# Kernel tuning notes

Hardware: AMD Instinct MI355X
Metric: run time of the kernel (lower is better)

## Reference

```python
import jax, jax.numpy as jnp
import numpy as np

PATCH = 16
HIDDEN = 1024
NUM_HEADS = 16
HEAD_DIM = HIDDEN // NUM_HEADS


def sinusoidal_pe(n, d):
    # standard transformer sinusoidal positional encoding, shape [n, d]
    pos = np.arange(n, dtype=np.float32)[:, None]
    i = np.arange(0, d, 2, dtype=np.float32)[None, :]
    ang = pos / np.power(10000.0, i / d)
    pe = np.zeros((n, d), dtype=np.float32)
    pe[:, 0::2] = np.sin(ang)
    pe[:, 1::2] = np.cos(ang)
    return jnp.asarray(pe)


def patch_embed(x, w, b):
    # Conv2d(kernel=stride=PATCH) == non-overlapping patch GEMM
    B, C, H, W = x.shape
    hp, wp = H // PATCH, W // PATCH
    xp = x.reshape(B, C, hp, PATCH, wp, PATCH)
    t = jnp.einsum('bchpwq,dcpq->bhwd', xp, w)  # [B, hp, wp, D]
    return t.reshape(B, hp * wp, -1) + b        # [B, N, D]


def _fit(x, w, b):
    t = patch_embed(x, w, b)
    t = t + sinusoidal_pe(t.shape[1], t.shape[2])
    B, N, _ = t.shape
    return t.reshape(B, N, NUM_HEADS, HEAD_DIM).transpose(0, 2, 1, 3)  # [B,H,N,hd]


def setup_inputs() -> dict:
    key = jax.random.key(0)
    ks = jax.random.split(key, 9)
    B, C, H, W = 16, 3, 512, 512
    return {
        'q_img': jax.random.normal(ks[0], (B, C, H, W), jnp.float32),
        'k_img': jax.random.normal(ks[1], (B, C, H, W), jnp.float32),
        'v_img': jax.random.normal(ks[2], (B, C, H, W), jnp.float32),
        'wq': jax.random.normal(ks[3], (HIDDEN, C, PATCH, PATCH), jnp.float32) * 0.02,
        'bq': jax.random.normal(ks[4], (HIDDEN,), jnp.float32) * 0.02,
        'wk': jax.random.normal(ks[5], (HIDDEN, C, PATCH, PATCH), jnp.float32) * 0.02,
        'bk': jax.random.normal(ks[6], (HIDDEN,), jnp.float32) * 0.02,
        'wv': jax.random.normal(ks[7], (HIDDEN, C, PATCH, PATCH), jnp.float32) * 0.02,
        'bv': jax.random.normal(ks[8], (HIDDEN,), jnp.float32) * 0.02,
    }


def reference(q_img, k_img, v_img, wq, bq, wk, bk, wv, bv):
    q = _fit(q_img, wq, bq)  # [B,H,N,hd]
    k = _fit(k_img, wk, bk)
    v = _fit(v_img, wv, bv)
    q = jax.nn.softmax(q, axis=-1)   # softmax over head_dim
    k = jax.nn.softmax(k, axis=-2)   # softmax over tokens
    scores = jnp.einsum('bhnd,bhne->bhde', k, v)   # k^T v : [B,H,hd,hd]
    ctx = jnp.einsum('bhnd,bhde->bhne', q, scores)  # [B,H,N,hd]
    B, h, N, hd = ctx.shape
    return ctx.transpose(0, 2, 1, 3).reshape(B, N, h * hd)  # [B,N,hidden]
```

## Files before the change

### kernel.cpp

```cpp
#include <hip/hip_runtime.h>
#include <hip/hip_bf16.h>


typedef float  f32x4  __attribute__((ext_vector_type(4)));
typedef __bf16 bf16x8 __attribute__((ext_vector_type(8)));

#define LN10000 9.210340371976184f

__device__ __forceinline__ unsigned short f2bf_bits(float f){
  union { float f; unsigned u; } a; a.f = f;
  unsigned r = a.u + 0x7FFFu + ((a.u >> 16) & 1u);
  return (unsigned short)(r >> 16);
}

__device__ __forceinline__ void gload16(const void* g, void* l){
  __builtin_amdgcn_global_load_lds((__attribute__((address_space(1))) void*)g,
                                   (__attribute__((address_space(3))) void*)l,
                                   16, 0, 0);
}


__global__ __launch_bounds__(256) void k_prep_w(
    const float* __restrict__ wq, const float* __restrict__ wk,
    const float* __restrict__ wv, unsigned short* __restrict__ wbf)
{
  int i = blockIdx.x*256 + threadIdx.x;
  if (i >= 589824) return;
  int z = i / 196608;
  int r = i - z*196608;
  const float* src = (z==0) ? wq : (z==1 ? wk : wv);
  f32x4 v = ((const f32x4*)src)[r];
  unsigned lo = (unsigned)f2bf_bits(v[0]) | ((unsigned)f2bf_bits(v[1]) << 16);
  unsigned hh = (unsigned)f2bf_bits(v[2]) | ((unsigned)f2bf_bits(v[3]) << 16);
  ((uint2*)wbf)[i] = make_uint2(lo, hh);
}

__global__ __launch_bounds__(256) void k_prep_pe(float* __restrict__ pe)
{
  int i = blockIdx.x*256 + threadIdx.x;
  if (i >= 1048576) return;
  int n = i >> 10, dd = i & 1023;
  float ex  = (float)(dd & ~1) * (1.0f/1024.0f);
  float ang = (float)n * expf(-LN10000 * ex);
  pe[i] = (dd & 1) ? cosf(ang) : sinf(ang);
}


__global__ __launch_bounds__(256, 2) void k_embed(
    const float* __restrict__ xq, const float* __restrict__ xk,
    const float* __restrict__ xv, const unsigned short* __restrict__ wbf,
    const float* __restrict__ bq, const float* __restrict__ bk,
    const float* __restrict__ bv, const float* __restrict__ pe,
    float* __restrict__ t_ws)
{
  __shared__ __align__(16) float          ldsA[128*64];
  __shared__ __align__(16) unsigned short ldsB[128*64];

  const int tid = threadIdx.x;
  int flat = blockIdx.x + (blockIdx.y << 3) + (blockIdx.z << 10);
  int orig = (flat & 7)*384 + (flat >> 3);
  const int z   = orig >> 10;
  const int rem = orig & 1023;
  const int m0  = (rem >> 3) * 128;
  const int d0  = (rem & 7) * 128;

  const float* x = (z==0) ? xq : (z==1 ? xk : xv);
  const unsigned short* wz = wbf + z*786432;
  const float* bias = (z==0) ? bq : (z==1 ? bk : bv);
  float* tout = t_ws + (size_t)z*16777216u;

  int aRow[8], aKK[8];
#pragma unroll
  for (int i=0;i<8;i++){
    int L   = i*4096 + tid*16;
    int row = L >> 8;
    int U   = L ^ ((row & 7) << 4);
    aKK[i]  = (U >> 2) & 63;
    int m   = m0 + row;
    int bimg = m >> 10, nt = m & 1023;
    aRow[i] = bimg*786432 + (nt>>5)*8192 + (nt&31)*16;
  }
  int bOff[4];
#pragma unroll
  for (int i=0;i<4;i++){
    int L   = i*4096 + tid*16;
    int row = L >> 7;
    int U   = L ^ ((row & 7) << 4);
    bOff[i] = (d0 + row)*768 + ((U >> 1) & 63);
  }

  const int lane = tid & 63;
  const int wid  = tid >> 6;
  const int ln   = lane & 15, hi4 = lane >> 4;
  const int wm   = wid >> 1,  wn  = wid & 1;

  f32x4 acc[4][4] = {};
  char* ldsAc = (char*)ldsA;
  char* ldsBc = (char*)ldsB;

  for (int ks=0; ks<12; ++ks){
#pragma unroll
    for (int i=0;i<8;i++){
      int k   = ks*64 + aKK[i];
      int c   = k >> 8, rem2 = k & 255;
      int goff = aRow[i] + c*262144 + (rem2>>4)*512 + (rem2 & 15);
      gload16(x + goff, ldsAc + i*4096 + wid*1024);
    }
#pragma unroll
    for (int i=0;i<4;i++){
      gload16(wz + bOff[i] + ks*64, ldsBc + i*4096 + wid*1024);
    }
    __syncthreads();

#pragma unroll
    for (int kc=0; kc<2; ++kc){
      bf16x8 af[4], bfr[4];
#pragma unroll
      for (int mi=0;mi<4;mi++){
        int row  = wm*64 + mi*16 + ln;
        int swz  = (row & 7) << 4;
        int base = row*256 + kc*128 + hi4*32;
        f32x4 lo = *(const f32x4*)(ldsAc + ( base        ^ swz));
        f32x4 hh = *(const f32x4*)(ldsAc + ((base + 16)  ^ swz));
        bf16x8 t;
        t[0]=(__bf16)lo[0]; t[1]=(__bf16)lo[1]; t[2]=(__bf16)lo[2]; t[3]=(__bf16)lo[3];
        t[4]=(__bf16)hh[0]; t[5]=(__bf16)hh[1]; t[6]=(__bf16)hh[2]; t[7]=(__bf16)hh[3];
        af[mi] = t;
      }
#pragma unroll
      for (int ni=0;ni<4;ni++){
        int row  = wn*64 + ni*16 + ln;
        int swz  = (row & 7) << 4;
        int base = row*128 + kc*64 + hi4*16;
        bfr[ni] = *(const bf16x8*)(ldsBc + (base ^ swz));
      }
#pragma unroll
      for (int mi=0;mi<4;mi++)
#pragma unroll
        for (int ni=0;ni<4;ni++)
          acc[mi][ni] = __builtin_amdgcn_mfma_f32_16x16x32_bf16(
              af[mi], bfr[ni], acc[mi][ni], 0, 0, 0);
    }
    __syncthreads();
  }

#pragma unroll
  for (int ni=0;ni<4;ni++){
    int dd = d0 + wn*64 + ni*16 + ln;
    float bv_ = bias[dd];
#pragma unroll
    for (int mi=0;mi<4;mi++){
#pragma unroll
      for (int r=0;r<4;r++){
        int m    = m0 + wm*64 + mi*16 + hi4*4 + r;
        int ntok = m & 1023;
        tout[(size_t)m*1024 + dd] = acc[mi][ni][r] + bv_ + pe[ntok*1024 + dd];
      }
    }
  }
}


__global__ __launch_bounds__(256) void k_scores(
    const float* __restrict__ t_ws, float* __restrict__ scoresRaw)
{
  __shared__ __align__(16) float lds[4][4096];
  __shared__ float ksumLds[4][64];

  const int tid = threadIdx.x;
  const int bh  = blockIdx.x;
  const int b   = bh >> 4, h = bh & 15;
  const float* kbase = t_ws + 16777216u + (size_t)b*1048576u + h*64;
  const float* vbase = t_ws + 33554432u + (size_t)b*1048576u + h*64;

  const int dq = tid & 15, eg = (tid>>4) & 3, npart = tid >> 6;
  const int r0   = tid >> 4;
  const int dcol = (tid & 15) * 4;

#define STAGE(BUF, CH) do{                                                \
    _Pragma("unroll")                                                     \
    for (int i=0;i<4;i++){                                                \
      int row = r0 + 16*i;                                                \
      size_t g = (size_t)((CH)*64 + row)*1024 + dcol;                     \
      f32x4 k4 = *(const f32x4*)(kbase + g);                              \
      f32x4 v4 = *(const f32x4*)(vbase + g);                              \
      f32x4 e;                                                            \
      e[0]=__expf(k4[0]); e[1]=__expf(k4[1]);                             \
      e[2]=__expf(k4[2]); e[3]=__expf(k4[3]);                             \
      *(f32x4*)(&lds[BUF][row*64 + dcol])     = e;                        \
      *(f32x4*)(&lds[2+(BUF)][row*64 + dcol]) = v4;                       \
    } }while(0)

  float acc[4][16] = {};
  float kp[4] = {0.f,0.f,0.f,0.f};

  STAGE(0, 0);
  __syncthreads();
  for (int ch=0; ch<16; ++ch){
    int cur = ch & 1;
    if (ch < 15) STAGE(cur^1, ch+1);
    for (int nn = npart; nn < 64; nn += 4){
      f32x4 ek4 = *(const f32x4*)(&lds[cur][nn*64 + dq*4]);
      f32x4 v0  = *(const f32x4*)(&lds[2+cur][nn*64 + eg*16 + 0]);
      f32x4 v1  = *(const f32x4*)(&lds[2+cur][nn*64 + eg*16 + 4]);
      f32x4 v2  = *(const f32x4*)(&lds[2+cur][nn*64 + eg*16 + 8]);
      f32x4 v3  = *(const f32x4*)(&lds[2+cur][nn*64 + eg*16 + 12]);
#pragma unroll
      for (int i2=0;i2<4;i2++){
        kp[i2] += ek4[i2];
#pragma unroll
        for (int j=0;j<4;j++){
          acc[i2][j+0]  += ek4[i2]*v0[j];
          acc[i2][j+4]  += ek4[i2]*v1[j];
          acc[i2][j+8]  += ek4[i2]*v2[j];
          acc[i2][j+12] += ek4[i2]*v3[j];
        }
      }
    }
    __syncthreads();
  }
#undef STAGE

  if (eg == 0){
#pragma unroll
    for (int i2=0;i2<4;i2++) ksumLds[npart][dq*4 + i2] = kp[i2];
  }

  float* pb = &lds[npart][0];
#pragma unroll
  for (int i2=0;i2<4;i2++){
    int base = (dq*4 + i2)*64 + eg*16;
    f32x4 a0; a0[0]=acc[i2][0];  a0[1]=acc[i2][1];  a0[2]=acc[i2][2];  a0[3]=acc[i2][3];
    f32x4 a1; a1[0]=acc[i2][4];  a1[1]=acc[i2][5];  a1[2]=acc[i2][6];  a1[3]=acc[i2][7];
    f32x4 a2; a2[0]=acc[i2][8];  a2[1]=acc[i2][9];  a2[2]=acc[i2][10]; a2[3]=acc[i2][11];
    f32x4 a3; a3[0]=acc[i2][12]; a3[1]=acc[i2][13]; a3[2]=acc[i2][14]; a3[3]=acc[i2][15];
    *(f32x4*)(pb + base + 0)  = a0;
    *(f32x4*)(pb + base + 4)  = a1;
    *(f32x4*)(pb + base + 8)  = a2;
    *(f32x4*)(pb + base + 12) = a3;
  }
  __syncthreads();

  float* outp = scoresRaw + (size_t)bh*4096;
#pragma unroll
  for (int i=0;i<4;i++){
    int q4 = (tid + 256*i)*4;
    int d  = q4 >> 6;
    float rk = 1.0f / (ksumLds[0][d] + ksumLds[1][d] + ksumLds[2][d] + ksumLds[3][d]);
    f32x4 s = *(const f32x4*)(&lds[0][q4]) + *(const f32x4*)(&lds[1][q4])
            + *(const f32x4*)(&lds[2][q4]) + *(const f32x4*)(&lds[3][q4]);
    s[0]*=rk; s[1]*=rk; s[2]*=rk; s[3]*=rk;
    *(f32x4*)(outp + q4) = s;
  }
}


__global__ __launch_bounds__(256) void k_ctx(
    const float* __restrict__ t_ws, const float* __restrict__ scoresRaw,
    float* __restrict__ out)
{
  __shared__ __align__(16) float S[64*64];
  __shared__ __align__(16) float qnT[64*132];

  const int tid   = threadIdx.x;
  const int bh    = blockIdx.y;
  const int b     = bh >> 4, h = bh & 15;
  const int chunk = blockIdx.x;
  const float* qbase = t_ws + (size_t)b*1048576u + h*64;

#pragma unroll
  for (int i=0;i<4;i++){
    int q4 = (tid + 256*i)*4;
    *(f32x4*)(S + q4) = *(const f32x4*)(scoresRaw + (size_t)bh*4096 + q4);
  }

  const int lane = tid & 63, w = tid >> 6;
  const int pos = lane & 15, rq = lane >> 4;
#pragma unroll
  for (int p=0;p<8;p++){
    int nl = w*32 + p*4 + rq;
    int n  = chunk*128 + nl;
    f32x4 qv = *(const f32x4*)(qbase + (size_t)n*1024 + pos*4);
    f32x4 e;
    e[0]=__expf(qv[0]); e[1]=__expf(qv[1]); e[2]=__expf(qv[2]); e[3]=__expf(qv[3]);
    float s = e[0]+e[1]+e[2]+e[3];
#pragma unroll
    for (int m2=1; m2<16; m2<<=1) s += __shfl_xor(s, m2);
    float r = 1.0f / s;
    qnT[(pos*4+0)*132 + nl] = e[0]*r;
    qnT[(pos*4+1)*132 + nl] = e[1]*r;
    qnT[(pos*4+2)*132 + nl] = e[2]*r;
    qnT[(pos*4+3)*132 + nl] = e[3]*r;
  }
  __syncthreads();

  const int eq = tid & 15, tg = tid >> 4;
  float acc[8][4] = {};
  for (int d=0; d<64; ++d){
    f32x4 s4 = *(const f32x4*)(S   + d*64  + eq*4);
    f32x4 q0 = *(const f32x4*)(qnT + d*132 + tg*8 + 0);
    f32x4 q1 = *(const f32x4*)(qnT + d*132 + tg*8 + 4);
#pragma unroll
    for (int j=0;j<4;j++){
      acc[0][j] += q0[0]*s4[j];
      acc[1][j] += q0[1]*s4[j];
      acc[2][j] += q0[2]*s4[j];
      acc[3][j] += q0[3]*s4[j];
      acc[4][j] += q1[0]*s4[j];
      acc[5][j] += q1[1]*s4[j];
      acc[6][j] += q1[2]*s4[j];
      acc[7][j] += q1[3]*s4[j];
    }
  }
#pragma unroll
  for (int i2=0;i2<8;i2++){
    int n = chunk*128 + tg*8 + i2;
    f32x4 o; o[0]=acc[i2][0]; o[1]=acc[i2][1]; o[2]=acc[i2][2]; o[3]=acc[i2][3];
    *(f32x4*)(out + (size_t)(b*1024 + n)*1024 + h*64 + eq*4) = o;
  }
}


extern "C" void kernel_launch(void* const* d_in, const int* in_sizes, int n_in,
                              void* d_out, int out_size, void* d_ws, size_t ws_size,
                              hipStream_t stream)
{
  const float* q_img = (const float*)d_in[0];
  const float* k_img = (const float*)d_in[1];
  const float* v_img = (const float*)d_in[2];
  const float* wq    = (const float*)d_in[3];
  const float* bq    = (const float*)d_in[4];
  const float* wk    = (const float*)d_in[5];
  const float* bk    = (const float*)d_in[6];
  const float* wv    = (const float*)d_in[7];
  const float* bv    = (const float*)d_in[8];
  float* out = (float*)d_out;
  char*  ws  = (char*)d_ws;

  float*          t_ws   = (float*)ws;
  unsigned short* wbf    = (unsigned short*)(ws + 0xC000000);
  float*          pe     = (float*)(ws + 0xC480000);
  float*          scores = (float*)(ws + 0xC880000);

  k_prep_w <<<dim3(2304), dim3(256), 0, stream>>>(wq, wk, wv, wbf);
  k_prep_pe<<<dim3(4096), dim3(256), 0, stream>>>(pe);
  k_embed  <<<dim3(8,128,3), dim3(256), 0, stream>>>(q_img,k_img,v_img, wbf,
                                                     bq,bk,bv, pe, t_ws);
  k_scores <<<dim3(256),  dim3(256), 0, stream>>>(t_ws, scores);
  k_ctx    <<<dim3(8,256), dim3(256), 0, stream>>>(t_ws, scores, out);
}
```

Before: 264.1 us.

## Convert A tile to bf16 at staging and double k_scores threads

In k_embed, the A operand is now loaded through registers and converted to bf16 before the LDS write, rather than being copied to LDS as fp32 by async loads and converted in the inner loop. This halves A's LDS footprint, which allows the occupancy hint to rise from 2 to 4 blocks per CU. The cost is losing the direct global-to-LDS load path and adding register pressure from the staged fp32 values. Separately, k_scores moves to 512 threads per block with a two-phase LDS reduction over eight token partitions, raising parallelism across the 256 blocks.

```diff
diff --git a/kernel.cpp b/kernel.cpp
--- a/kernel.cpp
+++ b/kernel.cpp
@@ -46,14 +46,14 @@
 }
 
 
-__global__ __launch_bounds__(256, 2) void k_embed(
+__global__ __launch_bounds__(256, 4) void k_embed(
     const float* __restrict__ xq, const float* __restrict__ xk,
     const float* __restrict__ xv, const unsigned short* __restrict__ wbf,
     const float* __restrict__ bq, const float* __restrict__ bk,
     const float* __restrict__ bv, const float* __restrict__ pe,
     float* __restrict__ t_ws)
 {
-  __shared__ __align__(16) float          ldsA[128*64];
+  __shared__ __align__(16) unsigned short ldsA[128*64];
   __shared__ __align__(16) unsigned short ldsB[128*64];
 
   const int tid = threadIdx.x;
@@ -69,16 +69,15 @@
   const float* bias = (z==0) ? bq : (z==1 ? bk : bv);
   float* tout = t_ws + (size_t)z*16777216u;
 
-  int aRow[8], aKK[8];
-#pragma unroll
-  for (int i=0;i<8;i++){
-    int L   = i*4096 + tid*16;
-    int row = L >> 8;
-    int U   = L ^ ((row & 7) << 4);
-    aKK[i]  = (U >> 2) & 63;
-    int m   = m0 + row;
-    int bimg = m >> 10, nt = m & 1023;
-    aRow[i] = bimg*786432 + (nt>>5)*8192 + (nt&31)*16;
+  const int slot = tid & 7;
+  const int rowb = tid >> 3;
+  int aRowG[4], aDst[4];
+#pragma unroll
+  for (int i=0;i<4;i++){
+    int row = i*32 + rowb;
+    int m = m0 + row, bimg = m >> 10, nt = m & 1023;
+    aRowG[i] = bimg*786432 + (nt>>5)*8192 + (nt&31)*16;
+    aDst[i]  = (row*128 + slot*16) ^ ((row & 7) << 4);
   }
   int bOff[4];
 #pragma unroll
@@ -99,17 +98,29 @@
   char* ldsBc = (char*)ldsB;
 
   for (int ks=0; ks<12; ++ks){
-#pragma unroll
-    for (int i=0;i<8;i++){
-      int k   = ks*64 + aKK[i];
-      int c   = k >> 8, rem2 = k & 255;
-      int goff = aRow[i] + c*262144 + (rem2>>4)*512 + (rem2 & 15);
-      gload16(x + goff, ldsAc + i*4096 + wid*1024);
+    int k0  = ks*64 + slot*8;
+    int c   = k0 >> 8, r2 = k0 & 255;
+    int koff = c*262144 + (r2>>4)*512 + (r2 & 15);
+    f32x4 a0[4], a1[4];
+#pragma unroll
+    for (int i=0;i<4;i++){
+      const float* g = x + aRowG[i] + koff;
+      a0[i] = *(const f32x4*)g;
+      a1[i] = *(const f32x4*)(g + 4);
     }
 #pragma unroll
     for (int i=0;i<4;i++){
       gload16(wz + bOff[i] + ks*64, ldsBc + i*4096 + wid*1024);
     }
+#pragma unroll
+    for (int i=0;i<4;i++){
+      bf16x8 t;
+      t[0]=(__bf16)a0[i][0]; t[1]=(__bf16)a0[i][1];
+      t[2]=(__bf16)a0[i][2]; t[3]=(__bf16)a0[i][3];
+      t[4]=(__bf16)a1[i][0]; t[5]=(__bf16)a1[i][1];
+      t[6]=(__bf16)a1[i][2]; t[7]=(__bf16)a1[i][3];
+      *(bf16x8*)(ldsAc + aDst[i]) = t;
+    }
     __syncthreads();
 
 #pragma unroll
@@ -118,21 +129,14 @@
 #pragma unroll
       for (int mi=0;mi<4;mi++){
         int row  = wm*64 + mi*16 + ln;
-        int swz  = (row & 7) << 4;
-        int base = row*256 + kc*128 + hi4*32;
-        f32x4 lo = *(const f32x4*)(ldsAc + ( base        ^ swz));
-        f32x4 hh = *(const f32x4*)(ldsAc + ((base + 16)  ^ swz));
-        bf16x8 t;
-        t[0]=(__bf16)lo[0]; t[1]=(__bf16)lo[1]; t[2]=(__bf16)lo[2]; t[3]=(__bf16)lo[3];
-        t[4]=(__bf16)hh[0]; t[5]=(__bf16)hh[1]; t[6]=(__bf16)hh[2]; t[7]=(__bf16)hh[3];
-        af[mi] = t;
+        int byte = (row*128 + kc*64 + hi4*16) ^ ((row & 7) << 4);
+        af[mi] = *(const bf16x8*)(ldsAc + byte);
       }
 #pragma unroll
       for (int ni=0;ni<4;ni++){
         int row  = wn*64 + ni*16 + ln;
-        int swz  = (row & 7) << 4;
-        int base = row*128 + kc*64 + hi4*16;
-        bfr[ni] = *(const bf16x8*)(ldsBc + (base ^ swz));
+        int byte = (row*128 + kc*64 + hi4*16) ^ ((row & 7) << 4);
+        bfr[ni] = *(const bf16x8*)(ldsBc + byte);
       }
 #pragma unroll
       for (int mi=0;mi<4;mi++)
@@ -161,11 +165,11 @@
 }
 
 
-__global__ __launch_bounds__(256) void k_scores(
-    const float* __restrict__ t_ws, float* __restrict__ scoresRaw)
+__global__ __launch_bounds__(512) void k_scores(
+    const float* __restrict__ t_ws, float* __restrict__ scoresOut)
 {
   __shared__ __align__(16) float lds[4][4096];
-  __shared__ float ksumLds[4][64];
+  __shared__ float ksumLds[8][64];
 
   const int tid = threadIdx.x;
   const int bh  = blockIdx.x;
@@ -179,8 +183,8 @@
 
 #define STAGE(BUF, CH) do{                                                \
     _Pragma("unroll")                                                     \
-    for (int i=0;i<4;i++){                                                \
-      int row = r0 + 16*i;                                                \
+    for (int i=0;i<2;i++){                                                \
+      int row = r0 + 32*i;                                                \
       size_t g = (size_t)((CH)*64 + row)*1024 + dcol;                     \
       f32x4 k4 = *(const f32x4*)(kbase + g);                              \
       f32x4 v4 = *(const f32x4*)(vbase + g);                              \
@@ -199,7 +203,7 @@
   for (int ch=0; ch<16; ++ch){
     int cur = ch & 1;
     if (ch < 15) STAGE(cur^1, ch+1);
-    for (int nn = npart; nn < 64; nn += 4){
+    for (int nn = npart; nn < 64; nn += 8){
       f32x4 ek4 = *(const f32x4*)(&lds[cur][nn*64 + dq*4]);
       f32x4 v0  = *(const f32x4*)(&lds[2+cur][nn*64 + eg*16 + 0]);
       f32x4 v1  = *(const f32x4*)(&lds[2+cur][nn*64 + eg*16 + 4]);
@@ -226,27 +230,46 @@
     for (int i2=0;i2<4;i2++) ksumLds[npart][dq*4 + i2] = kp[i2];
   }
 
-  float* pb = &lds[npart][0];
-#pragma unroll
-  for (int i2=0;i2<4;i2++){
-    int base = (dq*4 + i2)*64 + eg*16;
-    f32x4 a0; a0[0]=acc[i2][0];  a0[1]=acc[i2][1];  a0[2]=acc[i2][2];  a0[3]=acc[i2][3];
-    f32x4 a1; a1[0]=acc[i2][4];  a1[1]=acc[i2][5];  a1[2]=acc[i2][6];  a1[3]=acc[i2][7];
-    f32x4 a2; a2[0]=acc[i2][8];  a2[1]=acc[i2][9];  a2[2]=acc[i2][10]; a2[3]=acc[i2][11];
-    f32x4 a3; a3[0]=acc[i2][12]; a3[1]=acc[i2][13]; a3[2]=acc[i2][14]; a3[3]=acc[i2][15];
-    *(f32x4*)(pb + base + 0)  = a0;
-    *(f32x4*)(pb + base + 4)  = a1;
-    *(f32x4*)(pb + base + 8)  = a2;
-    *(f32x4*)(pb + base + 12) = a3;
+  if (npart < 4){
+    float* pb = &lds[npart][0];
+#pragma unroll
+    for (int i2=0;i2<4;i2++){
+      int base = (dq*4 + i2)*64 + eg*16;
+      f32x4 a0; a0[0]=acc[i2][0];  a0[1]=acc[i2][1];  a0[2]=acc[i2][2];  a0[3]=acc[i2][3];
+      f32x4 a1; a1[0]=acc[i2][4];  a1[1]=acc[i2][5];  a1[2]=acc[i2][6];  a1[3]=acc[i2][7];
+      f32x4 a2; a2[0]=acc[i2][8];  a2[1]=acc[i2][9];  a2[2]=acc[i2][10]; a2[3]=acc[i2][11];
+      f32x4 a3; a3[0]=acc[i2][12]; a3[1]=acc[i2][13]; a3[2]=acc[i2][14]; a3[3]=acc[i2][15];
+      *(f32x4*)(pb + base + 0)  = a0;
+      *(f32x4*)(pb + base + 4)  = a1;
+      *(f32x4*)(pb + base + 8)  = a2;
+      *(f32x4*)(pb + base + 12) = a3;
+    }
   }
   __syncthreads();
-
-  float* outp = scoresRaw + (size_t)bh*4096;
-#pragma unroll
-  for (int i=0;i<4;i++){
-    int q4 = (tid + 256*i)*4;
-    int d  = q4 >> 6;
-    float rk = 1.0f / (ksumLds[0][d] + ksumLds[1][d] + ksumLds[2][d] + ksumLds[3][d]);
+  if (npart >= 4){
+    float* pb = &lds[npart-4][0];
+#pragma unroll
+    for (int i2=0;i2<4;i2++){
+      int base = (dq*4 + i2)*64 + eg*16;
+#pragma unroll
+      for (int q=0;q<4;q++){
+        f32x4 cu = *(const f32x4*)(pb + base + 4*q);
+        cu[0]+=acc[i2][4*q+0]; cu[1]+=acc[i2][4*q+1];
+        cu[2]+=acc[i2][4*q+2]; cu[3]+=acc[i2][4*q+3];
+        *(f32x4*)(pb + base + 4*q) = cu;
+      }
+    }
+  }
+  __syncthreads();
+
+  float* outp = scoresOut + (size_t)bh*4096;
+#pragma unroll
+  for (int i=0;i<2;i++){
+    int idx = tid + 512*i;
+    int q4  = idx*4;
+    int d   = idx >> 4;
+    float rk = 1.0f / (ksumLds[0][d]+ksumLds[1][d]+ksumLds[2][d]+ksumLds[3][d]
+                      +ksumLds[4][d]+ksumLds[5][d]+ksumLds[6][d]+ksumLds[7][d]);
     f32x4 s = *(const f32x4*)(&lds[0][q4]) + *(const f32x4*)(&lds[1][q4])
             + *(const f32x4*)(&lds[2][q4]) + *(const f32x4*)(&lds[3][q4]);
     s[0]*=rk; s[1]*=rk; s[2]*=rk; s[3]*=rk;
@@ -256,7 +279,7 @@
 
 
 __global__ __launch_bounds__(256) void k_ctx(
-    const float* __restrict__ t_ws, const float* __restrict__ scoresRaw,
+    const float* __restrict__ t_ws, const float* __restrict__ scoresIn,
     float* __restrict__ out)
 {
   __shared__ __align__(16) float S[64*64];
@@ -271,7 +294,7 @@
 #pragma unroll
   for (int i=0;i<4;i++){
     int q4 = (tid + 256*i)*4;
-    *(f32x4*)(S + q4) = *(const f32x4*)(scoresRaw + (size_t)bh*4096 + q4);
+    *(f32x4*)(S + q4) = *(const f32x4*)(scoresIn + (size_t)bh*4096 + q4);
   }
 
   const int lane = tid & 63, w = tid >> 6;
@@ -346,6 +369,6 @@
   k_prep_pe<<<dim3(4096), dim3(256), 0, stream>>>(pe);
   k_embed  <<<dim3(8,128,3), dim3(256), 0, stream>>>(q_img,k_img,v_img, wbf,
                                                      bq,bk,bv, pe, t_ws);
-  k_scores <<<dim3(256),  dim3(256), 0, stream>>>(t_ws, scores);
+  k_scores <<<dim3(256),  dim3(512), 0, stream>>>(t_ws, scores);
   k_ctx    <<<dim3(8,256), dim3(256), 0, stream>>>(t_ws, scores, out);
 }
```

Result: slower. 318.1 us (+20.4%).
